# Kernel tuning notes

Hardware: AMD Instinct MI355X
Metric: run time of the kernel (lower is better)

The kernel has to match this reference:

```python
import jax, jax.numpy as jnp
import numpy as np

ALPHA = 0.5
SIGMA = 0.1
EPS = 1e-7
N, T = 8192, 512


def setup_inputs() -> dict:
    key = jax.random.key(0)
    k1, k2, k3 = jax.random.split(key, 3)
    logits = jax.random.normal(k1, (N, T), dtype=jnp.float32)
    pmf = jax.nn.softmax(logits, axis=-1)  # valid PMF rows
    times = jax.random.uniform(k2, (N,), dtype=jnp.float32, minval=0.0, maxval=float(T))
    events = jax.random.randint(k3, (N,), 0, 2).astype(jnp.int32)
    time_bins = jnp.arange(T, dtype=jnp.float32)
    return {"pmf": pmf, "times": times, "events": events, "time_bins": time_bins}


def reference(pmf, times, events, time_bins):
    n, t = pmf.shape
    # torch.bucketize(right=False) == searchsorted side='left'
    bin_idx = jnp.clip(jnp.searchsorted(time_bins, times, side='left') - 1, 0, t - 1)

    cdf = jnp.cumsum(pmf, axis=1)                 # (N, T)
    rows = jnp.arange(n)
    pmf_at = pmf[rows, bin_idx]                   # pmf[i, bin_idx[i]]
    cdf_at = cdf[rows, bin_idx]                   # cdf[i, bin_idx[i]]
    total = cdf[:, -1]
    surv = total - cdf_at + pmf_at                # sum pmf[i, bin_idx[i]:]

    nll = jnp.where(events == 1, -jnp.log(pmf_at + EPS), -jnp.log(surv + EPS))
    loss = nll.mean()

    # Pairwise ranking term (vectorized over event anchors i and later samples j)
    later = times[None, :] > times[:, None]       # later[i, j] = times[j] > times[i]
    cnt = later.sum(axis=1)                       # (N,) number of later samples per i
    G = cdf[:, bin_idx].T                         # G[i, j] = cdf[j, bin_idx[i]]
    e = jnp.exp((G - cdf_at[:, None]) / SIGMA)    # exp(diff / sigma)
    per_i = jnp.sum(jnp.where(later, e, 0.0), axis=1) / jnp.maximum(cnt, 1)
    valid = (events == 1) & (cnt > 0)
    n_pairs = valid.sum()
    rank_loss = jnp.sum(jnp.where(valid, per_i, 0.0))

    apply_rank = (events.sum() > 1) & (n_pairs > 0) & (ALPHA > 0)
    loss = jnp.where(apply_rank, loss + ALPHA * rank_loss / jnp.maximum(n_pairs, 1), loss)
    return loss
```

## Files before the change

kernel.cpp:

```cpp
#include <hip/hip_runtime.h>
#include <cstdint>
#include <cstddef>

#define SIGMA_INV 10.0f
#define EPS_C 1e-7f

constexpr int TDIM = 512;
constexpr int ROWS = 32;
constexpr int PITCH = 513;
constexpr int NB = 256;
constexpr int MAXC = 256;

__global__ __launch_bounds__(512) void rows_kernel(
    const float* __restrict__ pmf, const float* __restrict__ times,
    const int* __restrict__ events, const float* __restrict__ bins,
    float* __restrict__ SGTp, float* __restrict__ scaleA,
    float* __restrict__ einvA, int* __restrict__ kidxA,
    float* __restrict__ nll_part, int* __restrict__ ev_part, int N)
{
    __shared__ float lds[ROWS * PITCH];
    __shared__ float binsS[TDIM];
    __shared__ int karr[ROWS];
    __shared__ float nllv[ROWS];
    __shared__ int evv[ROWS];
    const int tid = threadIdx.x;
    const int lane = tid & 63;
    const int wid = tid >> 6;
    const int i0 = blockIdx.x * ROWS;

    binsS[tid] = bins[tid];

    float4 A[4][2];
    #pragma unroll
    for (int r = 0; r < 4; ++r) {
        const int i = i0 + wid * 4 + r;
        const float4* p4 = (const float4*)(pmf + (size_t)i * TDIM + lane * 8);
        A[r][0] = p4[0];
        A[r][1] = p4[1];
    }
    #pragma unroll
    for (int r = 0; r < 4; ++r) {
        const int rl = wid * 4 + r;
        float c0 = A[r][0].x, c1 = c0 + A[r][0].y, c2 = c1 + A[r][0].z, c3 = c2 + A[r][0].w;
        float c4 = c3 + A[r][1].x, c5 = c4 + A[r][1].y, c6 = c5 + A[r][1].z, c7 = c6 + A[r][1].w;
        float v = c7;
        #pragma unroll
        for (int d = 1; d < 64; d <<= 1) {
            float u = __shfl_up(v, d);
            if (lane >= d) v += u;
        }
        const float excl = v - c7;
        const int base = rl * PITCH + lane * 8;
        lds[base + 0] = c0 + excl; lds[base + 1] = c1 + excl;
        lds[base + 2] = c2 + excl; lds[base + 3] = c3 + excl;
        lds[base + 4] = c4 + excl; lds[base + 5] = c5 + excl;
        lds[base + 6] = c6 + excl; lds[base + 7] = c7 + excl;
    }
    __syncthreads();

    if (tid < ROWS) {
        const int i = i0 + tid;
        const float t = times[i];
        int lo = 0, hi = TDIM;
        while (lo < hi) {
            int mid = (lo + hi) >> 1;
            if (binsS[mid] < t) lo = mid + 1; else hi = mid;
        }
        int k = lo - 1;
        k = k < 0 ? 0 : (k > TDIM - 1 ? TDIM - 1 : k);
        const float cdf_at = lds[tid * PITCH + k];
        const float tot = lds[tid * PITCH + (TDIM - 1)];
        const float pmf_at = pmf[(size_t)i * TDIM + k];
        const float surv = tot - cdf_at + pmf_at;
        nllv[tid] = (events[i] == 1) ? -logf(pmf_at + EPS_C) : -logf(surv + EPS_C);
        evv[tid] = events[i];
        scaleA[i] = expf(-cdf_at * SIGMA_INV);
        einvA[i] = expf(cdf_at * SIGMA_INV);
        kidxA[i] = k;
        karr[tid] = k;
    }
    __syncthreads();

    float acc = 0.f;
    #pragma unroll
    for (int s = 0; s < ROWS; ++s) {
        const float c = lds[s * PITCH + tid];
        if (tid < karr[s]) acc += expf(c * SIGMA_INV);
    }
    SGTp[(size_t)blockIdx.x * TDIM + tid] = acc;

    if (wid == 0) {
        float nv = (lane < ROWS) ? nllv[lane] : 0.f;
        int ev = (lane < ROWS) ? evv[lane] : 0;
        #pragma unroll
        for (int d = 32; d > 0; d >>= 1) {
            nv += __shfl_down(nv, d);
            ev += __shfl_down(ev, d);
        }
        if (lane == 0) { nll_part[blockIdx.x] = nv; ev_part[blockIdx.x] = ev; }
    }
}

__global__ __launch_bounds__(256) void bucket_kernel(
    const float* __restrict__ SGTp, const float* __restrict__ times,
    const int* __restrict__ events, const int* __restrict__ kidx,
    const float* __restrict__ scaleA, const float* __restrict__ einvA,
    float* __restrict__ rank_part, int* __restrict__ npair_part, int N)
{
    __shared__ float red[4];
    __shared__ int redi[4];
    __shared__ int cj[MAXC], oj[MAXC];
    __shared__ float mt[MAXC], me[MAXC];
    __shared__ int ncl_sh;
    __shared__ float SGT_sh;
    __shared__ int CGT_sh;

    const int k = blockIdx.x;
    const int tid = threadIdx.x;
    const int lane = tid & 63;
    const int wid = tid >> 6;

    if (tid == 0) ncl_sh = 0;
    __syncthreads();

    float sv = SGTp[(size_t)tid * TDIM + k];
    #pragma unroll
    for (int d = 32; d > 0; d >>= 1) sv += __shfl_down(sv, d);
    if (lane == 0) red[wid] = sv;

    int cnt = 0;
    const int4* kx4 = (const int4*)kidx;
    for (int ch = tid; ch < N / 4; ch += 256) {
        const int4 kx = kx4[ch];
        const int j0 = ch * 4;
        cnt += (kx.x > k) + (kx.y > k) + (kx.z > k) + (kx.w > k);
        if (kx.x == k) { int p = atomicAdd(&ncl_sh, 1); if (p < MAXC) cj[p] = j0 + 0; }
        if (kx.y == k) { int p = atomicAdd(&ncl_sh, 1); if (p < MAXC) cj[p] = j0 + 1; }
        if (kx.z == k) { int p = atomicAdd(&ncl_sh, 1); if (p < MAXC) cj[p] = j0 + 2; }
        if (kx.w == k) { int p = atomicAdd(&ncl_sh, 1); if (p < MAXC) cj[p] = j0 + 3; }
    }
    #pragma unroll
    for (int d = 32; d > 0; d >>= 1) cnt += __shfl_down(cnt, d);
    if (lane == 0) redi[wid] = cnt;
    __syncthreads();
    if (tid == 0) {
        SGT_sh = (red[0] + red[1]) + (red[2] + red[3]);
        CGT_sh = redi[0] + redi[1] + redi[2] + redi[3];
    }
    __syncthreads();

    const int nc = ncl_sh < MAXC ? ncl_sh : MAXC;
    if (tid < nc) {
        const int myj = cj[tid];
        int r = 0;
        for (int m = 0; m < nc; ++m) r += (cj[m] < myj) ? 1 : 0;
        oj[r] = myj;
    }
    __syncthreads();
    if (tid < nc) { mt[tid] = times[oj[tid]]; me[tid] = einvA[oj[tid]]; }
    __syncthreads();

    float pi = 0.f;
    int vf = 0;
    if (tid < nc) {
        const int i = oj[tid];
        const float ti = mt[tid];
        float s = 0.f;
        int c = 0;
        for (int m = 0; m < nc; ++m) {
            if (mt[m] > ti) { s += me[m]; c++; }
        }
        const int C = CGT_sh + c;
        if (events[i] == 1 && C > 0) {
            vf = 1;
            pi = scaleA[i] * (SGT_sh + s) / (float)C;
        }
    }
    #pragma unroll
    for (int d = 32; d > 0; d >>= 1) {
        pi += __shfl_down(pi, d);
        vf += __shfl_down(vf, d);
    }
    __syncthreads();
    if (lane == 0) { red[wid] = pi; redi[wid] = vf; }
    __syncthreads();
    if (tid == 0) {
        rank_part[k] = (red[0] + red[1]) + (red[2] + red[3]);
        npair_part[k] = redi[0] + redi[1] + redi[2] + redi[3];
    }
}

__global__ __launch_bounds__(512) void final_kernel(
    const float* __restrict__ nll_part, const int* __restrict__ ev_part,
    const float* __restrict__ rank_part, const int* __restrict__ npair_part,
    float* __restrict__ out, int N)
{
    __shared__ double s1[512];
    __shared__ double s2[512];
    __shared__ int i1[512];
    __shared__ int i2[512];
    const int t = threadIdx.x;
    s1[t] = (t < NB) ? (double)nll_part[t] : 0.0;
    i2[t] = (t < NB) ? ev_part[t] : 0;
    s2[t] = (double)rank_part[t];
    i1[t] = npair_part[t];
    __syncthreads();
    for (int off = 256; off > 0; off >>= 1) {
        if (t < off) {
            s1[t] += s1[t + off];
            s2[t] += s2[t + off];
            i1[t] += i1[t + off];
            i2[t] += i2[t + off];
        }
        __syncthreads();
    }
    if (t == 0) {
        double loss = s1[0] / (double)N;
        if (i2[0] > 1 && i1[0] > 0) loss += 0.5 * s2[0] / (double)i1[0];
        out[0] = (float)loss;
    }
}

extern "C" void kernel_launch(void* const* d_in, const int* in_sizes, int n_in,
                              void* d_out, int out_size, void* d_ws, size_t ws_size,
                              hipStream_t stream) {
    const float* pmf = (const float*)d_in[0];
    const float* times = (const float*)d_in[1];
    const int* events = (const int*)d_in[2];
    const float* bins = (const float*)d_in[3];
    const int N = in_sizes[1];

    float* SGTp = (float*)d_ws;
    float* scaleA = SGTp + (size_t)NB * TDIM;
    float* einvA = scaleA + N;
    float* nll_part = einvA + N;
    float* rank_part = nll_part + NB;
    int* kidxA = (int*)(rank_part + TDIM);
    int* ev_part = kidxA + N;
    int* npair_part = ev_part + NB;

    rows_kernel<<<N / ROWS, 512, 0, stream>>>(pmf, times, events, bins,
                                              SGTp, scaleA, einvA, kidxA,
                                              nll_part, ev_part, N);
    bucket_kernel<<<TDIM, 256, 0, stream>>>(SGTp, times, events, kidxA,
                                            scaleA, einvA,
                                            rank_part, npair_part, N);
    final_kernel<<<1, 512, 0, stream>>>(nll_part, ev_part, rank_part,
                                        npair_part, (float*)d_out, N);
}
```

Measured before the change: 26.68 us.

## Fuse three kernels into one persistent kernel with grid barrier and last-block reduction

Merges the row-scan, per-bucket ranking and final reduction kernels into one launch of 512 blocks of 16 rows each. An atomic-counter grid barrier separates the phases, and the last block to finish performs the final reduction. The aim is to remove two kernel launch gaps and the tail idle time between dependent kernels. In exchange it needs a memset per call, relies on all 512 blocks being co-resident (otherwise the spin barrier deadlocks), and halves rows per block in the first phase.

```diff
diff --git a/kernel.cpp b/kernel.cpp
--- a/kernel.cpp
+++ b/kernel.cpp
@@ -6,41 +6,51 @@
 #define EPS_C 1e-7f
 
 constexpr int TDIM = 512;
-constexpr int ROWS = 32;
+constexpr int ROWS2 = 16;
 constexpr int PITCH = 513;
-constexpr int NB = 256;
+constexpr int NBLK = 512;
 constexpr int MAXC = 256;
 
-__global__ __launch_bounds__(512) void rows_kernel(
+__global__ __launch_bounds__(512, 4) void fused_kernel(
     const float* __restrict__ pmf, const float* __restrict__ times,
     const int* __restrict__ events, const float* __restrict__ bins,
+    unsigned* __restrict__ counters,
     float* __restrict__ SGTp, float* __restrict__ scaleA,
     float* __restrict__ einvA, int* __restrict__ kidxA,
-    float* __restrict__ nll_part, int* __restrict__ ev_part, int N)
+    float* __restrict__ nll_part, int* __restrict__ ev_part,
+    float* __restrict__ rank_part, int* __restrict__ npair_part,
+    float* __restrict__ out, int N)
 {
-    __shared__ float lds[ROWS * PITCH];
+    __shared__ __align__(16) char smem[ROWS2 * PITCH * 4];
     __shared__ float binsS[TDIM];
-    __shared__ int karr[ROWS];
-    __shared__ float nllv[ROWS];
-    __shared__ int evv[ROWS];
+    __shared__ int karr[ROWS2];
+    __shared__ float nllv[ROWS2];
+    __shared__ int evv[ROWS2];
+    __shared__ int ncl_sh;
+    __shared__ float SGT_sh;
+    __shared__ int CGT_sh;
+    __shared__ int last_sh;
+
+    float* tile = (float*)smem;
     const int tid = threadIdx.x;
     const int lane = tid & 63;
     const int wid = tid >> 6;
-    const int i0 = blockIdx.x * ROWS;
+    const int b = blockIdx.x;
+    const int i0 = b * ROWS2;
 
     binsS[tid] = bins[tid];
 
-    float4 A[4][2];
-    #pragma unroll
-    for (int r = 0; r < 4; ++r) {
-        const int i = i0 + wid * 4 + r;
+    float4 A[2][2];
+    #pragma unroll
+    for (int r = 0; r < 2; ++r) {
+        const int i = i0 + wid * 2 + r;
         const float4* p4 = (const float4*)(pmf + (size_t)i * TDIM + lane * 8);
         A[r][0] = p4[0];
         A[r][1] = p4[1];
     }
     #pragma unroll
-    for (int r = 0; r < 4; ++r) {
-        const int rl = wid * 4 + r;
+    for (int r = 0; r < 2; ++r) {
+        const int rl = wid * 2 + r;
         float c0 = A[r][0].x, c1 = c0 + A[r][0].y, c2 = c1 + A[r][0].z, c3 = c2 + A[r][0].w;
         float c4 = c3 + A[r][1].x, c5 = c4 + A[r][1].y, c6 = c5 + A[r][1].z, c7 = c6 + A[r][1].w;
         float v = c7;
@@ -50,15 +60,13 @@
             if (lane >= d) v += u;
         }
         const float excl = v - c7;
-        const int base = rl * PITCH + lane * 8;
-        lds[base + 0] = c0 + excl; lds[base + 1] = c1 + excl;
-        lds[base + 2] = c2 + excl; lds[base + 3] = c3 + excl;
-        lds[base + 4] = c4 + excl; lds[base + 5] = c5 + excl;
-        lds[base + 6] = c6 + excl; lds[base + 7] = c7 + excl;
-    }
-    __syncthreads();
-
-    if (tid < ROWS) {
+        float* t = tile + rl * PITCH + lane * 8;
+        t[0] = c0 + excl; t[1] = c1 + excl; t[2] = c2 + excl; t[3] = c3 + excl;
+        t[4] = c4 + excl; t[5] = c5 + excl; t[6] = c6 + excl; t[7] = c7 + excl;
+    }
+    __syncthreads();
+
+    if (tid < ROWS2) {
         const int i = i0 + tid;
         const float t = times[i];
         int lo = 0, hi = TDIM;
@@ -68,8 +76,8 @@
         }
         int k = lo - 1;
         k = k < 0 ? 0 : (k > TDIM - 1 ? TDIM - 1 : k);
-        const float cdf_at = lds[tid * PITCH + k];
-        const float tot = lds[tid * PITCH + (TDIM - 1)];
+        const float cdf_at = tile[tid * PITCH + k];
+        const float tot = tile[tid * PITCH + (TDIM - 1)];
         const float pmf_at = pmf[(size_t)i * TDIM + k];
         const float surv = tot - cdf_at + pmf_at;
         nllv[tid] = (events[i] == 1) ? -logf(pmf_at + EPS_C) : -logf(surv + EPS_C);
@@ -83,42 +91,44 @@
 
     float acc = 0.f;
     #pragma unroll
-    for (int s = 0; s < ROWS; ++s) {
-        const float c = lds[s * PITCH + tid];
+    for (int s = 0; s < ROWS2; ++s) {
+        const float c = tile[s * PITCH + tid];
         if (tid < karr[s]) acc += expf(c * SIGMA_INV);
     }
-    SGTp[(size_t)blockIdx.x * TDIM + tid] = acc;
+    SGTp[(size_t)b * TDIM + tid] = acc;
 
     if (wid == 0) {
-        float nv = (lane < ROWS) ? nllv[lane] : 0.f;
-        int ev = (lane < ROWS) ? evv[lane] : 0;
-        #pragma unroll
-        for (int d = 32; d > 0; d >>= 1) {
+        float nv = (lane < ROWS2) ? nllv[lane] : 0.f;
+        int ev = (lane < ROWS2) ? evv[lane] : 0;
+        #pragma unroll
+        for (int d = 8; d > 0; d >>= 1) {
             nv += __shfl_down(nv, d);
             ev += __shfl_down(ev, d);
         }
-        if (lane == 0) { nll_part[blockIdx.x] = nv; ev_part[blockIdx.x] = ev; }
-    }
-}
-
-__global__ __launch_bounds__(256) void bucket_kernel(
-    const float* __restrict__ SGTp, const float* __restrict__ times,
-    const int* __restrict__ events, const int* __restrict__ kidx,
-    const float* __restrict__ scaleA, const float* __restrict__ einvA,
-    float* __restrict__ rank_part, int* __restrict__ npair_part, int N)
-{
-    __shared__ float red[4];
-    __shared__ int redi[4];
-    __shared__ int cj[MAXC], oj[MAXC];
-    __shared__ float mt[MAXC], me[MAXC];
-    __shared__ int ncl_sh;
-    __shared__ float SGT_sh;
-    __shared__ int CGT_sh;
-
-    const int k = blockIdx.x;
-    const int tid = threadIdx.x;
-    const int lane = tid & 63;
-    const int wid = tid >> 6;
+        if (lane == 0) { nll_part[b] = nv; ev_part[b] = ev; }
+    }
+
+    __syncthreads();
+    if (tid == 0) {
+        __threadfence();
+        __hip_atomic_fetch_add(&counters[0], 1u, __ATOMIC_ACQ_REL,
+                               __HIP_MEMORY_SCOPE_AGENT);
+        while (__hip_atomic_load(&counters[0], __ATOMIC_ACQUIRE,
+                                 __HIP_MEMORY_SCOPE_AGENT) < (unsigned)NBLK) {
+            __builtin_amdgcn_s_sleep(8);
+        }
+    }
+    __syncthreads();
+
+    const int k = b;
+    int* cj = (int*)smem;
+    int* oj = cj + MAXC;
+    float* mt = (float*)(oj + MAXC);
+    float* me = mt + MAXC;
+    float* redf = me + MAXC;
+    float* red2f = redf + 8;
+    int* redi = (int*)(red2f + 8);
+    int* red2i = redi + 8;
 
     if (tid == 0) ncl_sh = 0;
     __syncthreads();
@@ -126,11 +136,13 @@
     float sv = SGTp[(size_t)tid * TDIM + k];
     #pragma unroll
     for (int d = 32; d > 0; d >>= 1) sv += __shfl_down(sv, d);
-    if (lane == 0) red[wid] = sv;
+    if (lane == 0) redf[wid] = sv;
 
     int cnt = 0;
-    const int4* kx4 = (const int4*)kidx;
-    for (int ch = tid; ch < N / 4; ch += 256) {
+    const int4* kx4 = (const int4*)kidxA;
+    #pragma unroll
+    for (int it = 0; it < 4; ++it) {
+        const int ch = it * 512 + tid;
         const int4 kx = kx4[ch];
         const int j0 = ch * 4;
         cnt += (kx.x > k) + (kx.y > k) + (kx.z > k) + (kx.w > k);
@@ -144,8 +156,10 @@
     if (lane == 0) redi[wid] = cnt;
     __syncthreads();
     if (tid == 0) {
-        SGT_sh = (red[0] + red[1]) + (red[2] + red[3]);
-        CGT_sh = redi[0] + redi[1] + redi[2] + redi[3];
+        float s8 = 0.f; int c8 = 0;
+        #pragma unroll
+        for (int w = 0; w < 8; ++w) { s8 += redf[w]; c8 += redi[w]; }
+        SGT_sh = s8; CGT_sh = c8;
     }
     __syncthreads();
 
@@ -181,43 +195,48 @@
         pi += __shfl_down(pi, d);
         vf += __shfl_down(vf, d);
     }
-    __syncthreads();
-    if (lane == 0) { red[wid] = pi; redi[wid] = vf; }
-    __syncthreads();
-    if (tid == 0) {
-        rank_part[k] = (red[0] + red[1]) + (red[2] + red[3]);
-        npair_part[k] = redi[0] + redi[1] + redi[2] + redi[3];
-    }
-}
-
-__global__ __launch_bounds__(512) void final_kernel(
-    const float* __restrict__ nll_part, const int* __restrict__ ev_part,
-    const float* __restrict__ rank_part, const int* __restrict__ npair_part,
-    float* __restrict__ out, int N)
-{
-    __shared__ double s1[512];
-    __shared__ double s2[512];
-    __shared__ int i1[512];
-    __shared__ int i2[512];
-    const int t = threadIdx.x;
-    s1[t] = (t < NB) ? (double)nll_part[t] : 0.0;
-    i2[t] = (t < NB) ? ev_part[t] : 0;
-    s2[t] = (double)rank_part[t];
-    i1[t] = npair_part[t];
-    __syncthreads();
-    for (int off = 256; off > 0; off >>= 1) {
-        if (t < off) {
-            s1[t] += s1[t + off];
-            s2[t] += s2[t + off];
-            i1[t] += i1[t + off];
-            i2[t] += i2[t + off];
-        }
+    if (lane == 0) { red2f[wid] = pi; red2i[wid] = vf; }
+    __syncthreads();
+    if (tid == 0) {
+        float s8 = 0.f; int c8 = 0;
+        #pragma unroll
+        for (int w = 0; w < 8; ++w) { s8 += red2f[w]; c8 += red2i[w]; }
+        rank_part[k] = s8;
+        npair_part[k] = c8;
+    }
+
+    __syncthreads();
+    if (tid == 0) {
+        __threadfence();
+        unsigned old = __hip_atomic_fetch_add(&counters[1], 1u, __ATOMIC_ACQ_REL,
+                                              __HIP_MEMORY_SCOPE_AGENT);
+        last_sh = (old == (unsigned)(NBLK - 1)) ? 1 : 0;
+    }
+    __syncthreads();
+    if (last_sh) {
+        double* sd1 = (double*)smem;
+        double* sd2 = sd1 + 512;
+        int* si1 = (int*)(sd2 + 512);
+        int* si2 = si1 + 512;
+        sd1[tid] = (double)nll_part[tid];
+        sd2[tid] = (double)rank_part[tid];
+        si1[tid] = npair_part[tid];
+        si2[tid] = ev_part[tid];
         __syncthreads();
-    }
-    if (t == 0) {
-        double loss = s1[0] / (double)N;
-        if (i2[0] > 1 && i1[0] > 0) loss += 0.5 * s2[0] / (double)i1[0];
-        out[0] = (float)loss;
+        for (int off = 256; off > 0; off >>= 1) {
+            if (tid < off) {
+                sd1[tid] += sd1[tid + off];
+                sd2[tid] += sd2[tid + off];
+                si1[tid] += si1[tid + off];
+                si2[tid] += si2[tid + off];
+            }
+            __syncthreads();
+        }
+        if (tid == 0) {
+            double loss = sd1[0] / (double)N;
+            if (si2[0] > 1 && si1[0] > 0) loss += 0.5 * sd2[0] / (double)si1[0];
+            out[0] = (float)loss;
+        }
     }
 }
 
@@ -230,21 +249,19 @@
     const float* bins = (const float*)d_in[3];
     const int N = in_sizes[1];
 
-    float* SGTp = (float*)d_ws;
-    float* scaleA = SGTp + (size_t)NB * TDIM;
+    char* ws = (char*)d_ws;
+    unsigned* counters = (unsigned*)ws;
+    float* SGTp = (float*)(ws + 256);
+    float* scaleA = SGTp + (size_t)NBLK * TDIM;
     float* einvA = scaleA + N;
     float* nll_part = einvA + N;
-    float* rank_part = nll_part + NB;
+    float* rank_part = nll_part + NBLK;
     int* kidxA = (int*)(rank_part + TDIM);
     int* ev_part = kidxA + N;
-    int* npair_part = ev_part + NB;
-
-    rows_kernel<<<N / ROWS, 512, 0, stream>>>(pmf, times, events, bins,
-                                              SGTp, scaleA, einvA, kidxA,
-                                              nll_part, ev_part, N);
-    bucket_kernel<<<TDIM, 256, 0, stream>>>(SGTp, times, events, kidxA,
-                                            scaleA, einvA,
-                                            rank_part, npair_part, N);
-    final_kernel<<<1, 512, 0, stream>>>(nll_part, ev_part, rank_part,
-                                        npair_part, (float*)d_out, N);
+    int* npair_part = ev_part + NBLK;
+
+    hipMemsetAsync(counters, 0, 2 * sizeof(unsigned), stream);
+    fused_kernel<<<NBLK, 512, 0, stream>>>(
+        pmf, times, events, bins, counters, SGTp, scaleA, einvA, kidxA,
+        nll_part, ev_part, rank_part, npair_part, (float*)d_out, N);
 }
```

After: 69.04 us. 2.59x slower.
